# Performance work log

Measured on AMD Instinct MI355X. Metric: run time of the kernel, lower is better.

The kernel has to match this reference:

```python
import jax, jax.numpy as jnp
import numpy as np


def setup_inputs() -> dict:
    key = jax.random.key(0)
    k1, k2 = jax.random.split(key)
    x = jax.random.normal(k1, (16, 2048, 256), dtype=jnp.float32)
    embed = jax.random.normal(k2, (1024, 256), dtype=jnp.float32)
    return {"x": x, "embed": embed}


def reference(x, embed):
    shape = x.shape
    xf = x.reshape(-1, shape[-1])  # (N, d)
    dist = -(jnp.sum(xf * xf, axis=1, keepdims=True)
             - 2.0 * (xf @ embed.T)
             + jnp.sum(embed * embed, axis=1)[None, :])  # (N, K)
    embed_ind = jnp.argmax(dist, axis=-1)  # (N,)
    embed_ind = embed_ind.reshape(shape[:-1])  # (B, T)
    quantize = embed[embed_ind]  # (B, T, d) gather
    return quantize, embed_ind
```

## Files before the change

### kernel.cpp

```cpp
#include <hip/hip_runtime.h>
#include <stdint.h>

#define NROWS 32768
#define DIMS  256
#define KCB   1024
#define BM 128
#define BN 128
#define GY (KCB/BN)
#define MARGIN 0.25f
#define CROWS 32

typedef _Float16 half8   __attribute__((ext_vector_type(8)));
typedef float    f32x4   __attribute__((ext_vector_type(4)));
typedef short    short4v __attribute__((ext_vector_type(4)));
typedef short    short8v __attribute__((ext_vector_type(8)));

__device__ __forceinline__ void gload_lds16(const void* g, void* l) {
    __builtin_amdgcn_global_load_lds(
        (const __attribute__((address_space(1))) uint32_t*)g,
        (__attribute__((address_space(3))) uint32_t*)l, 16, 0, 0);
}

__device__ __forceinline__ short f16h(float v) {
    _Float16 hh = (_Float16)v;
    return __builtin_bit_cast(short, hh);
}

__global__ __launch_bounds__(256) void xsplit(const float* __restrict__ x,
                                              short* __restrict__ Xh) {
    int T = blockIdx.x * 256 + threadIdx.x;
    int l = T & 63, c = (T >> 6) & 7, G = T >> 9;
    int row = G * 16 + (l & 15);
    int kb  = c * 32 + (l >> 4) * 8;
    const f32x4* src = (const f32x4*)(x + (size_t)row * DIMS + kb);
    f32x4 a = src[0], b = src[1];
    short8v h;
    #pragma unroll
    for (int e = 0; e < 4; ++e) { h[e] = f16h(a[e]); h[4 + e] = f16h(b[e]); }
    *(short8v*)(Xh + (size_t)G * 4096 + c * 512 + l * 8) = h;
}

__global__ __launch_bounds__(256) void esplit(const float* __restrict__ embed,
                                              short* __restrict__ Eh,
                                              float* __restrict__ he2) {
    int r = blockIdx.x * 4 + (threadIdx.x >> 6);
    int l = threadIdx.x & 63;
    f32x4 v = ((const f32x4*)(embed + (size_t)r * DIMS))[l];
    float s = v[0]*v[0] + v[1]*v[1] + v[2]*v[2] + v[3]*v[3];
    #pragma unroll
    for (int off = 32; off > 0; off >>= 1) s += __shfl_down(s, off, 64);
    if (l == 0) he2[r] = 0.5f * s;
    int G = r >> 4, cc = l >> 3;
    int fl = (r & 15) + 16 * ((l >> 1) & 3);
    size_t base = (size_t)G * 4096 + cc * 512 + fl * 8 + (l & 1) * 4;
    short4v h;
    #pragma unroll
    for (int e = 0; e < 4; ++e) h[e] = f16h(v[e]);
    *(short4v*)(Eh + base) = h;
}

__global__ __launch_bounds__(256, 4) void vq_mfma(
    const short* __restrict__ Xh, const short* __restrict__ Eh,
    const float* __restrict__ he2, float4* __restrict__ part)
{
    __shared__ char  lds[32768];
    __shared__ float sarr[BM * 2];
    __shared__ int   iarr[BM * 2];
    __shared__ float barr[BM * 2];

    const int t = threadIdx.x, lane = t & 63, w = t >> 6;
    const int wm = w >> 1, wn = w & 1;
    const int sid = blockIdx.x;
    const int xcd = sid & 7, j = sid >> 3;
    const int rb = xcd * 32 + (j >> 3), cb = j & 7;
    const int rowBase = rb * BM, colBase = cb * BN;

    const char* gA[4];
    const char* gB[4];
    #pragma unroll
    for (int m = 0; m < 4; ++m)
        gA[m] = (const char*)Xh + (size_t)(rb * 8 + wm * 4 + m) * 8192 + lane * 16;
    #pragma unroll
    for (int n = 0; n < 4; ++n)
        gB[n] = (const char*)Eh + (size_t)(cb * 8 + wn * 4 + n) * 8192 + lane * 16;
    char* lw = lds + w * 8192;

    f32x4 acc[4][4];
    #pragma unroll
    for (int m = 0; m < 4; ++m)
        #pragma unroll
        for (int n = 0; n < 4; ++n) acc[m][n] = (f32x4){0.f, 0.f, 0.f, 0.f};

    #pragma unroll
    for (int m = 0; m < 4; ++m) gload_lds16(gA[m], lw + m * 1024);
    #pragma unroll
    for (int n = 0; n < 4; ++n) gload_lds16(gB[n], lw + 4096 + n * 1024);

    #pragma unroll
    for (int c = 0; c < 8; ++c) {
        asm volatile("s_waitcnt vmcnt(0)" ::: "memory");
        __builtin_amdgcn_sched_barrier(0);

        half8 A[4], B[4];
        #pragma unroll
        for (int m = 0; m < 4; ++m)
            A[m] = *(const half8*)(lw + m * 1024 + lane * 16);
        #pragma unroll
        for (int n = 0; n < 4; ++n)
            B[n] = *(const half8*)(lw + 4096 + n * 1024 + lane * 16);
        asm volatile("s_waitcnt lgkmcnt(0)" ::: "memory");
        __builtin_amdgcn_sched_barrier(0);

        if (c < 7) {
            #pragma unroll
            for (int m = 0; m < 4; ++m)
                gload_lds16(gA[m] + (c + 1) * 1024, lw + m * 1024);
            #pragma unroll
            for (int n = 0; n < 4; ++n)
                gload_lds16(gB[n] + (c + 1) * 1024, lw + 4096 + n * 1024);
        }
        __builtin_amdgcn_sched_barrier(0);

        __builtin_amdgcn_s_setprio(1);
        #pragma unroll
        for (int m = 0; m < 4; ++m)
            #pragma unroll
            for (int n = 0; n < 4; ++n)
                acc[m][n] = __builtin_amdgcn_mfma_f32_16x16x32_f16(A[m], B[n], acc[m][n], 0, 0, 0);
        __builtin_amdgcn_s_setprio(0);
    }

    float h2[4];
    const int c15 = lane & 15;
    #pragma unroll
    for (int n = 0; n < 4; ++n) h2[n] = he2[colBase + 64 * wn + 16 * n + c15];
    const int colg0 = colBase + 64 * wn + c15;

    #pragma unroll
    for (int m = 0; m < 4; ++m) {
        #pragma unroll
        for (int reg = 0; reg < 4; ++reg) {
            float b1 = acc[m][0][reg] - h2[0];
            int   i1 = colg0;
            float b2 = -3.4e38f;
            #pragma unroll
            for (int n = 1; n < 4; ++n) {
                float s = acc[m][n][reg] - h2[n];
                if (s > b1) { b2 = b1; b1 = s; i1 = colg0 + 16 * n; }
                else        { b2 = fmaxf(b2, s); }
            }
            #pragma unroll
            for (int msk = 1; msk <= 8; msk <<= 1) {
                float ob1 = __shfl_xor(b1, msk, 64);
                int   oi1 = __shfl_xor(i1, msk, 64);
                float ob2 = __shfl_xor(b2, msk, 64);
                if (ob1 > b1 || (ob1 == b1 && oi1 < i1)) {
                    b2 = fmaxf(b1, ob2); b1 = ob1; i1 = oi1;
                } else {
                    b2 = fmaxf(b2, ob1);
                }
            }
            if (c15 == 0) {
                int row = 64 * wm + 16 * m + 4 * (lane >> 4) + reg;
                sarr[row * 2 + wn] = b1;
                iarr[row * 2 + wn] = i1;
                barr[row * 2 + wn] = b2;
            }
        }
    }
    __syncthreads();
    if (t < BM) {
        float s0 = sarr[t*2], s1 = sarr[t*2+1];
        int   i0 = iarr[t*2], i1 = iarr[t*2+1];
        float c0 = barr[t*2], c1 = barr[t*2+1];
        float b1, b2; int bi;
        if (s1 > s0) { b1 = s1; bi = i1; b2 = fmaxf(s0, c1); }
        else         { b1 = s0; bi = i0; b2 = fmaxf(s1, c0); }
        part[(size_t)(rowBase + t) * GY + cb] =
            make_float4(b1, __int_as_float(bi), b2, 0.f);
    }
}

__device__ __forceinline__ float dot16(f32x4 xa, f32x4 xb, f32x4 xc, f32x4 xd,
                                       const float* __restrict__ erow, int q) {
    const f32x4* er = (const f32x4*)(erow + q * 16);
    f32x4 ea = er[0], eb = er[1], ec = er[2], ed = er[3];
    float s = xa[0] * ea[0];
    s = fmaf(xa[1], ea[1], s); s = fmaf(xa[2], ea[2], s); s = fmaf(xa[3], ea[3], s);
    s = fmaf(xb[0], eb[0], s); s = fmaf(xb[1], eb[1], s);
    s = fmaf(xb[2], eb[2], s); s = fmaf(xb[3], eb[3], s);
    s = fmaf(xc[0], ec[0], s); s = fmaf(xc[1], ec[1], s);
    s = fmaf(xc[2], ec[2], s); s = fmaf(xc[3], ec[3], s);
    s = fmaf(xd[0], ed[0], s); s = fmaf(xd[1], ed[1], s);
    s = fmaf(xd[2], ed[2], s); s = fmaf(xd[3], ed[3], s);
    s += __shfl_xor(s, 1, 64);
    s += __shfl_xor(s, 2, 64);
    s += __shfl_xor(s, 4, 64);
    s += __shfl_xor(s, 8, 64);
    return s;
}

__global__ __launch_bounds__(256) void vq_combine(
    const float4* __restrict__ part, const float* __restrict__ embed,
    const float* __restrict__ x, const float* __restrict__ he2,
    float* __restrict__ outq, float* __restrict__ outi)
{
    __shared__ int idxS[CROWS];
    __shared__ int flagL[CROWS];
    __shared__ int flagN;
    const int t = threadIdx.x, l = t & 63, w = t >> 6;
    const int rowBase = blockIdx.x * CROWS;

    if (t == 0) flagN = 0;
    __syncthreads();

    if (t < CROWS) {
        const int row = rowBase + t;
        float4 p = part[(size_t)row * GY];
        float b1 = p.x; int i1 = __float_as_int(p.y); float b2 = p.z;
        #pragma unroll
        for (int g = 1; g < GY; ++g) {
            float4 q = part[(size_t)row * GY + g];
            float c1 = q.x; int j1 = __float_as_int(q.y); float c2 = q.z;
            if (c1 > b1 || (c1 == b1 && j1 < i1)) { b2 = fmaxf(b1, c2); b1 = c1; i1 = j1; }
            else                                  { b2 = fmaxf(b2, c1); }
        }
        idxS[t] = i1;
        outi[row] = (float)i1;
        if (b1 - b2 < MARGIN) {
            int s = atomicAdd(&flagN, 1);
            flagL[s] = t;
        }
    }
    __syncthreads();

    #pragma unroll
    for (int qq = 0; qq < (CROWS * 64) / 256; ++qq) {
        int f = t + 256 * qq;
        int r = f >> 6, c4 = f & 63;
        int e = idxS[r];
        f32x4 v = *(const f32x4*)(embed + (size_t)e * DIMS + c4 * 4);
        *(f32x4*)(outq + (size_t)(rowBase + r) * DIMS + c4 * 4) = v;
    }
    __syncthreads();

    const int nf = flagN;
    const int q = l & 15, pgrp = l >> 4;
    for (int it = w; it < nf; it += 4) {
        int rrow = rowBase + flagL[it];
        const f32x4* xr = (const f32x4*)(x + (size_t)rrow * DIMS + q * 16);
        f32x4 xa = xr[0], xb = xr[1], xc = xr[2], xd = xr[3];

        float4 pc[GY];
        #pragma unroll
        for (int g = 0; g < GY; ++g) pc[g] = part[(size_t)rrow * GY + g];
        float B1 = pc[0].x;
        #pragma unroll
        for (int g = 1; g < GY; ++g) B1 = fmaxf(B1, pc[g].x);
        const float T = B1 - MARGIN;

        float wb = -3.4e38f; int wi = 0x7fffffff;
        #pragma unroll
        for (int g = 0; g < GY; ++g) {
            if (pc[g].z >= T) {
                #pragma unroll 2
                for (int i = 0; i < BN / 4; ++i) {
                    int code = g * BN + i * 4 + pgrp;
                    float s = dot16(xa, xb, xc, xd,
                                    embed + (size_t)code * DIMS, q) - he2[code];
                    if (s > wb || (s == wb && code < wi)) { wb = s; wi = code; }
                }
            } else if (pc[g].x >= T) {
                int code = __float_as_int(pc[g].y);
                float s = dot16(xa, xb, xc, xd,
                                embed + (size_t)code * DIMS, q) - he2[code];
                if (s > wb || (s == wb && code < wi)) { wb = s; wi = code; }
            }
        }
        #pragma unroll
        for (int msk = 16; msk <= 32; msk <<= 1) {
            float ob = __shfl_xor(wb, msk, 64);
            int   oi = __shfl_xor(wi, msk, 64);
            if (ob > wb || (ob == wb && oi < wi)) { wb = ob; wi = oi; }
        }
        f32x4 v = ((const f32x4*)(embed + (size_t)wi * DIMS))[l];
        ((f32x4*)(outq + (size_t)rrow * DIMS))[l] = v;
        if (l == 0) outi[rrow] = (float)wi;
    }
}

extern "C" void kernel_launch(void* const* d_in, const int* in_sizes, int n_in,
                              void* d_out, int out_size, void* d_ws, size_t ws_size,
                              hipStream_t stream) {
    const float* x     = (const float*)d_in[0];
    const float* embed = (const float*)d_in[1];
    char* ws = (char*)d_ws;
    float*  he2  = (float*)ws;
    float4* part = (float4*)(ws + 8192);
    short*  Xh   = (short*)(ws + 8192 + 4194304);
    short*  Eh   = (short*)(ws + 8192 + 4194304 + 16777216);
    float*  out  = (float*)d_out;
    float*  outi = out + (size_t)NROWS * DIMS;

    xsplit<<<4096, 256, 0, stream>>>(x, Xh);
    esplit<<<KCB / 4, 256, 0, stream>>>(embed, Eh, he2);
    vq_mfma<<<(NROWS / BM) * GY, 256, 0, stream>>>(Xh, Eh, he2, part);
    vq_combine<<<NROWS / CROWS, 256, 0, stream>>>(part, embed, x, he2, out, outi);
}
```

Measured before the change: 84.66 us.

## Load MFMA operands directly from global into registers with double buffering

Replaces the per-wave global-to-LDS staging (global_load_lds plus explicit waitcnts) with direct global loads into register fragments, double-buffered across two register sets so loads for chunk c+2 overlap MFMAs on chunk c. This removes LDS traffic, the LDS allocation and the manual wait barriers. Register pressure rises, so launch bounds drop to 3 waves per SIMD, and compiler-inserted waits may serialize differently.

```diff
diff --git a/kernel.cpp b/kernel.cpp
--- a/kernel.cpp
+++ b/kernel.cpp
@@ -14,12 +14,6 @@
 typedef float    f32x4   __attribute__((ext_vector_type(4)));
 typedef short    short4v __attribute__((ext_vector_type(4)));
 typedef short    short8v __attribute__((ext_vector_type(8)));
-
-__device__ __forceinline__ void gload_lds16(const void* g, void* l) {
-    __builtin_amdgcn_global_load_lds(
-        (const __attribute__((address_space(1))) uint32_t*)g,
-        (__attribute__((address_space(3))) uint32_t*)l, 16, 0, 0);
-}
 
 __device__ __forceinline__ short f16h(float v) {
     _Float16 hh = (_Float16)v;
@@ -59,11 +53,10 @@
     *(short4v*)(Eh + base) = h;
 }
 
-__global__ __launch_bounds__(256, 4) void vq_mfma(
+__global__ __launch_bounds__(256, 3) void vq_mfma(
     const short* __restrict__ Xh, const short* __restrict__ Eh,
     const float* __restrict__ he2, float4* __restrict__ part)
 {
-    __shared__ char  lds[32768];
     __shared__ float sarr[BM * 2];
     __shared__ int   iarr[BM * 2];
     __shared__ float barr[BM * 2];
@@ -75,60 +68,47 @@
     const int rb = xcd * 32 + (j >> 3), cb = j & 7;
     const int rowBase = rb * BM, colBase = cb * BN;
 
-    const char* gA[4];
-    const char* gB[4];
+    const char* baseA = (const char*)Xh + (size_t)(rb * 8 + wm * 4) * 8192 + lane * 16;
+    const char* baseB = (const char*)Eh + (size_t)(cb * 8 + wn * 4) * 8192 + lane * 16;
+
+    f32x4 acc[4][4];
     #pragma unroll
     for (int m = 0; m < 4; ++m)
-        gA[m] = (const char*)Xh + (size_t)(rb * 8 + wm * 4 + m) * 8192 + lane * 16;
-    #pragma unroll
-    for (int n = 0; n < 4; ++n)
-        gB[n] = (const char*)Eh + (size_t)(cb * 8 + wn * 4 + n) * 8192 + lane * 16;
-    char* lw = lds + w * 8192;
-
-    f32x4 acc[4][4];
-    #pragma unroll
-    for (int m = 0; m < 4; ++m)
         #pragma unroll
         for (int n = 0; n < 4; ++n) acc[m][n] = (f32x4){0.f, 0.f, 0.f, 0.f};
 
-    #pragma unroll
-    for (int m = 0; m < 4; ++m) gload_lds16(gA[m], lw + m * 1024);
-    #pragma unroll
-    for (int n = 0; n < 4; ++n) gload_lds16(gB[n], lw + 4096 + n * 1024);
-
-    #pragma unroll
-    for (int c = 0; c < 8; ++c) {
-        asm volatile("s_waitcnt vmcnt(0)" ::: "memory");
-        __builtin_amdgcn_sched_barrier(0);
-
-        half8 A[4], B[4];
-        #pragma unroll
-        for (int m = 0; m < 4; ++m)
-            A[m] = *(const half8*)(lw + m * 1024 + lane * 16);
-        #pragma unroll
-        for (int n = 0; n < 4; ++n)
-            B[n] = *(const half8*)(lw + 4096 + n * 1024 + lane * 16);
-        asm volatile("s_waitcnt lgkmcnt(0)" ::: "memory");
-        __builtin_amdgcn_sched_barrier(0);
-
-        if (c < 7) {
-            #pragma unroll
-            for (int m = 0; m < 4; ++m)
-                gload_lds16(gA[m] + (c + 1) * 1024, lw + m * 1024);
-            #pragma unroll
-            for (int n = 0; n < 4; ++n)
-                gload_lds16(gB[n] + (c + 1) * 1024, lw + 4096 + n * 1024);
-        }
-        __builtin_amdgcn_sched_barrier(0);
-
-        __builtin_amdgcn_s_setprio(1);
-        #pragma unroll
-        for (int m = 0; m < 4; ++m)
-            #pragma unroll
-            for (int n = 0; n < 4; ++n)
-                acc[m][n] = __builtin_amdgcn_mfma_f32_16x16x32_f16(A[m], B[n], acc[m][n], 0, 0, 0);
-        __builtin_amdgcn_s_setprio(0);
-    }
+#define LOADC(Ab, Bb, CC)                                                     \
+    {                                                                         \
+        _Pragma("unroll")                                                     \
+        for (int m = 0; m < 4; ++m)                                           \
+            Ab[m] = *(const half8*)(baseA + m * 8192 + (CC) * 1024);          \
+        _Pragma("unroll")                                                     \
+        for (int n = 0; n < 4; ++n)                                           \
+            Bb[n] = *(const half8*)(baseB + n * 8192 + (CC) * 1024);          \
+    }
+#define DOMFMA(Ab, Bb)                                                        \
+    {                                                                         \
+        _Pragma("unroll")                                                     \
+        for (int m = 0; m < 4; ++m)                                           \
+            _Pragma("unroll")                                                 \
+            for (int n = 0; n < 4; ++n)                                       \
+                acc[m][n] = __builtin_amdgcn_mfma_f32_16x16x32_f16(           \
+                    Ab[m], Bb[n], acc[m][n], 0, 0, 0);                        \
+    }
+
+    half8 A0[4], B0[4], A1[4], B1[4];
+    LOADC(A0, B0, 0)
+    LOADC(A1, B1, 1)
+    DOMFMA(A0, B0)  LOADC(A0, B0, 2)
+    DOMFMA(A1, B1)  LOADC(A1, B1, 3)
+    DOMFMA(A0, B0)  LOADC(A0, B0, 4)
+    DOMFMA(A1, B1)  LOADC(A1, B1, 5)
+    DOMFMA(A0, B0)  LOADC(A0, B0, 6)
+    DOMFMA(A1, B1)  LOADC(A1, B1, 7)
+    DOMFMA(A0, B0)
+    DOMFMA(A1, B1)
+#undef LOADC
+#undef DOMFMA
 
     float h2[4];
     const int c15 = lane & 15;
```

Measured after the change: 91.97 us. 1.09x slower.
